# Kernel optimization log

Hardware: AMD Instinct MI355X
Metric: run time of the kernel (lower is better)

The kernel has to match this reference:

```python
import jax, jax.numpy as jnp
import numpy as np

Q_LORA = 1536
KV_LORA = 512
ROPE_DIM = 64
NOPE_DIM = 128
NUM_HEADS = 16
QK_HEAD_DIM = NOPE_DIM + ROPE_DIM  # 192
HEAD_SIZE = KV_LORA + ROPE_DIM     # 576
MAX_POS = 4096
ROPE_BASE = 10000.0
T = 32768


def _rope_cos_sin(positions):
    # inv_freq: [ROPE_DIM//2]
    inv_freq = 1.0 / (ROPE_BASE ** (jnp.arange(0, ROPE_DIM, 2, dtype=jnp.float32) / ROPE_DIM))
    freqs = positions.astype(jnp.float32)[:, None] * inv_freq[None, :]  # [T, D/2]
    return jnp.cos(freqs), jnp.sin(freqs)


def _apply_rope_neox(x, cos, sin):
    # x: [T, H, D]; cos/sin: [T, D/2] broadcast over heads
    x1, x2 = jnp.split(x, 2, axis=-1)
    c = cos[:, None, :]
    s = sin[:, None, :]
    return jnp.concatenate([x1 * c - x2 * s, x2 * c + x1 * s], axis=-1)


def setup_inputs() -> dict:
    key = jax.random.key(0)
    k1, k2, k3 = jax.random.split(key, 3)
    qkv_lora = jax.random.normal(k1, (T, Q_LORA + KV_LORA + ROPE_DIM), dtype=jnp.float32)
    positions = jax.random.randint(k2, (T,), 0, MAX_POS, dtype=jnp.int64)
    Wq = jax.random.normal(k3, (Q_LORA, NUM_HEADS * QK_HEAD_DIM), dtype=jnp.float32) * 0.02
    kv_cache = jnp.zeros((T, HEAD_SIZE), dtype=jnp.float32)
    slot_mapping = jnp.arange(T, dtype=jnp.int64)
    return {"qkv_lora": qkv_lora, "positions": positions, "Wq": Wq,
            "kv_cache": kv_cache, "slot_mapping": slot_mapping}


def reference(qkv_lora, positions, Wq, kv_cache, slot_mapping):
    # split low-rank projections
    q_c = qkv_lora[:, :Q_LORA]                               # [T, 1536]
    kv_c = qkv_lora[:, Q_LORA:Q_LORA + KV_LORA]              # [T, 512]
    k_pe = qkv_lora[:, Q_LORA + KV_LORA:]                    # [T, 64]

    # q_b_proj GEMM then reshape to heads
    q = (q_c @ Wq).reshape(T, NUM_HEADS, QK_HEAD_DIM)        # [T, H, 192]

    # RoPE on q rope slice and k_pe (neox style)
    cos, sin = _rope_cos_sin(positions)
    q_pe = _apply_rope_neox(q[..., NOPE_DIM:], cos, sin)     # [T, H, 64]
    k_pe_rot = _apply_rope_neox(k_pe[:, None, :], cos, sin)  # [T, 1, 64]
    q = jnp.concatenate([q[..., :NOPE_DIM], q_pe], axis=-1)

    # paged KV cache scatter write: concat(kv_c, k_pe) at slot_mapping
    entry = jnp.concatenate([kv_c, k_pe_rot[:, 0, :]], axis=-1)  # [T, 576]
    kv_cache = kv_cache.at[slot_mapping].set(entry)

    return q, kv_c, k_pe_rot, kv_cache
```

## Files before the change

kernel.cpp:

```cpp
#include <hip/hip_runtime.h>
#include <hip/hip_bf16.h>
#include <stdint.h>

typedef unsigned short ushort_t;
typedef __attribute__((ext_vector_type(4))) float f32x4;
typedef __attribute__((ext_vector_type(8))) short short8;

#define T_TOK 32768
#define QL    1536
#define KVL   512
#define RD    64
#define NQ    3072
#define ROWW  2112
#define HS    576

#define BM 256
#define BN 256
#define BK 64
#define KT (QL / BK)
#define MT (T_TOK / BM)
#define NT (NQ / BN)

#define NLOG (-0.28782313662425572f)

static __device__ __forceinline__ short f2bf(float x) {
  __hip_bfloat16 h = __float2bfloat16(x);
  return *reinterpret_cast<short*>(&h);
}

#define GLOAD16(gp, lp)                                        \
  __builtin_amdgcn_global_load_lds(                            \
      (const __attribute__((address_space(1))) void*)(gp),     \
      (__attribute__((address_space(3))) void*)(lp), 16, 0, 0)

__global__ __launch_bounds__(256) void aconv_kernel(const float* __restrict__ qkv,
                                                    ushort_t* __restrict__ Abf) {
  int g = blockIdx.x * 256 + threadIdx.x;
  int row = g / 192;
  int col = (g - row * 192) * 8;
  const float* s = qkv + (size_t)row * ROWW + col;
  f32x4 a = *(const f32x4*)s;
  f32x4 b = *(const f32x4*)(s + 4);
  short8 v;
  v[0] = f2bf(a[0]); v[1] = f2bf(a[1]); v[2] = f2bf(a[2]); v[3] = f2bf(a[3]);
  v[4] = f2bf(b[0]); v[5] = f2bf(b[1]); v[6] = f2bf(b[2]); v[7] = f2bf(b[3]);
  *(short8*)(Abf + (size_t)row * QL + col) = v;
}

__global__ void wq_t_kernel(const float* __restrict__ Wq, ushort_t* __restrict__ Wt) {
  __shared__ float tile[32][33];
  int tx = threadIdx.x, ty = threadIdx.y;
  int n0 = blockIdx.x * 32, k0 = blockIdx.y * 32;
#pragma unroll
  for (int j = 0; j < 32; j += 8)
    tile[ty + j][tx] = Wq[(size_t)(k0 + ty + j) * NQ + n0 + tx];
  __syncthreads();
#pragma unroll
  for (int j = 0; j < 32; j += 8)
    Wt[(size_t)(n0 + ty + j) * QL + k0 + tx] = f2bf(tile[tx][ty + j]);
}

__global__ __launch_bounds__(512, 2) void gemm_rope_kernel(
    const ushort_t* __restrict__ Abf, const int* __restrict__ pos,
    const ushort_t* __restrict__ wt, float* __restrict__ out_q) {
  __shared__ ushort_t lds[2][2][2][256 * 32];

  int bid = blockIdx.x;
  int vb = (bid & 7) * (MT * NT / 8) + (bid >> 3);
  int m0 = (vb / NT) * BM;
  int n0 = (vb % NT) * BN;

  int tid = threadIdx.x;
  int wv = tid >> 6, ln = tid & 63;
  int l16 = ln & 15, lq4 = ln >> 4;
  int wm = wv >> 2, wn = wv & 3;

  int srow = wv * 32 + (ln >> 2);
  int schunk = ((ln & 3) ^ ((ln >> 3) & 3)) * 8;
  const ushort_t* aS = Abf + (size_t)(m0 + srow) * QL + schunk;
  const ushort_t* bS = wt  + (size_t)(n0 + srow) * QL + schunk;
  int sdst = wv * 32 * 32;

#define STG(PAR, AB, KH, TT, SRC) do {                                         \
    GLOAD16((SRC) + (size_t)(TT) * BK + (KH) * 32,           &lds[PAR][AB][KH][sdst]);       \
    GLOAD16((SRC) + (size_t)(TT) * BK + (KH) * 32 + 16 * QL, &lds[PAR][AB][KH][sdst + 512]); \
  } while (0)

  int rkey = (l16 >> 1) & 3;
  int aoff = (wm * 128 + l16) * 32 + (lq4 ^ rkey) * 8;
  int boff = (wn * 64  + l16) * 32 + (lq4 ^ rkey) * 8;

  f32x4 acc[8][4];
#pragma unroll
  for (int i = 0; i < 8; ++i)
#pragma unroll
    for (int j = 0; j < 4; ++j) acc[i][j] = (f32x4)0.0f;

  STG(0, 0, 0, 0, aS);
  STG(0, 1, 0, 0, bS);
  STG(0, 0, 1, 0, aS);
  STG(0, 1, 1, 0, bS);
  STG(1, 0, 0, 1, aS);
  STG(1, 1, 0, 1, bS);

#define CLUSTER(ACCBASE, AF, BF)                                               \
  __builtin_amdgcn_s_setprio(1);                                               \
  _Pragma("unroll")                                                            \
  for (int q = 0; q < 4; ++q)                                                  \
    _Pragma("unroll")                                                          \
    for (int n = 0; n < 4; ++n)                                                \
      acc[(ACCBASE) + q][n] = __builtin_amdgcn_mfma_f32_16x16x32_bf16(         \
          AF[q], BF[n], acc[(ACCBASE) + q][n], 0, 0, 0);                       \
  __builtin_amdgcn_s_setprio(0);

#pragma unroll 2
  for (int t = 0; t < KT; ++t) {
    int par = t & 1;
    const ushort_t* Ak0 = &lds[par][0][0][0];
    const ushort_t* Bk0 = &lds[par][1][0][0];
    const ushort_t* Ak1 = &lds[par][0][1][0];
    const ushort_t* Bk1 = &lds[par][1][1][0];
    short8 af0[4], af1[4], bf0[4], ag0[4], ag1[4], bg0[4];

    __builtin_amdgcn_sched_barrier(0);
    if (t == KT - 1) { asm volatile("s_waitcnt vmcnt(0)" ::: "memory"); }
    else             { asm volatile("s_waitcnt vmcnt(4)" ::: "memory"); }
    __builtin_amdgcn_s_barrier();
    __builtin_amdgcn_sched_barrier(0);

#pragma unroll
    for (int q = 0; q < 4; ++q) af0[q] = *(const short8*)(Ak0 + aoff + q * 512);
#pragma unroll
    for (int n = 0; n < 4; ++n) bf0[n] = *(const short8*)(Bk0 + boff + n * 512);
#pragma unroll
    for (int q = 0; q < 4; ++q) af1[q] = *(const short8*)(Ak0 + aoff + (4 + q) * 512);
    if (t + 1 < KT) { STG(par ^ 1, 0, 1, t + 1, aS); STG(par ^ 1, 1, 1, t + 1, bS); }
#pragma unroll
    for (int q = 0; q < 4; ++q) ag0[q] = *(const short8*)(Ak1 + aoff + q * 512);
#pragma unroll
    for (int n = 0; n < 4; ++n) bg0[n] = *(const short8*)(Bk1 + boff + n * 512);
#pragma unroll
    for (int q = 0; q < 4; ++q) ag1[q] = *(const short8*)(Ak1 + aoff + (4 + q) * 512);
    __builtin_amdgcn_sched_barrier(0);

    CLUSTER(0, af0, bf0)
    CLUSTER(4, af1, bf0)

    __builtin_amdgcn_s_barrier();
    __builtin_amdgcn_sched_barrier(0);
    if (t + 2 < KT) { STG(par, 0, 0, t + 2, aS); STG(par, 1, 0, t + 2, bS); }

    CLUSTER(0, ag0, bg0)
    CLUSTER(4, ag1, bg0)
  }

  int gn = n0 + wn * 64;
  bool ropew = ((gn % 192) == 128);
  if (!ropew) {
#pragma unroll
    for (int mi = 0; mi < 8; ++mi)
#pragma unroll
      for (int r = 0; r < 4; ++r) {
        int t = m0 + wm * 128 + mi * 16 + lq4 * 4 + r;
        float* rowp = out_q + (size_t)t * NQ + gn + l16;
        rowp[0]  = acc[mi][0][r];
        rowp[16] = acc[mi][1][r];
        rowp[32] = acc[mi][2][r];
        rowp[48] = acc[mi][3][r];
      }
  } else {
    float invf0 = __expf((float)l16 * NLOG);
    float invf1 = __expf((float)(l16 + 16) * NLOG);
#pragma unroll
    for (int mi = 0; mi < 8; ++mi)
#pragma unroll
      for (int r = 0; r < 4; ++r) {
        int t = m0 + wm * 128 + mi * 16 + lq4 * 4 + r;
        float p = (float)pos[t];
        float s0, c0, s1, c1;
        __sincosf(p * invf0, &s0, &c0);
        __sincosf(p * invf1, &s1, &c1);
        float x1a = acc[mi][0][r], x1b = acc[mi][1][r];
        float x2a = acc[mi][2][r], x2b = acc[mi][3][r];
        float* rowp = out_q + (size_t)t * NQ + gn + l16;
        rowp[0]  = x1a * c0 - x2a * s0;
        rowp[16] = x1b * c1 - x2b * s1;
        rowp[32] = x2a * c0 + x1a * s0;
        rowp[48] = x2b * c1 + x1b * s1;
      }
  }
}

__global__ void kv_kernel(const float* __restrict__ qkv, const int* __restrict__ pos,
                          const int* __restrict__ slots,
                          float* __restrict__ out_kvc, float* __restrict__ out_kpe,
                          float* __restrict__ out_cache) {
  int tok = blockIdx.x * 4 + (threadIdx.x >> 6);
  int lane = threadIdx.x & 63;
  const float* src = qkv + (size_t)tok * ROWW + QL;
  float* dkv = out_kvc + (size_t)tok * KVL;
  int slot = slots[tok];
  float* dc = out_cache + (size_t)slot * HS;
#pragma unroll
  for (int i = 0; i < 2; ++i) {
    f32x4 v = *(const f32x4*)(src + (size_t)(lane + 64 * i) * 4);
    *(f32x4*)(dkv + (size_t)(lane + 64 * i) * 4) = v;
    *(f32x4*)(dc + (size_t)(lane + 64 * i) * 4) = v;
  }
  if (lane < 32) {
    float x1 = src[KVL + lane], x2 = src[KVL + 32 + lane];
    float p = (float)pos[tok];
    float invf = __expf((float)lane * NLOG);
    float s, c;
    __sincosf(p * invf, &s, &c);
    float r1 = x1 * c - x2 * s;
    float r2 = x2 * c + x1 * s;
    out_kpe[(size_t)tok * RD + lane] = r1;
    out_kpe[(size_t)tok * RD + 32 + lane] = r2;
    dc[KVL + lane] = r1;
    dc[KVL + 32 + lane] = r2;
  }
}

extern "C" void kernel_launch(void* const* d_in, const int* in_sizes, int n_in,
                              void* d_out, int out_size, void* d_ws, size_t ws_size,
                              hipStream_t stream) {
  const float* qkv       = (const float*)d_in[0];
  const int*   positions = (const int*)d_in[1];
  const float* Wq        = (const float*)d_in[2];
  const int*   slots     = (const int*)d_in[4];

  float* out_q     = (float*)d_out;
  float* out_kvc   = out_q   + (size_t)T_TOK * NQ;
  float* out_kpe   = out_kvc + (size_t)T_TOK * KVL;
  float* out_cache = out_kpe + (size_t)T_TOK * RD;

  size_t abf_bytes = (size_t)T_TOK * QL * sizeof(ushort_t);
  size_t wt_bytes  = (size_t)NQ * QL * sizeof(ushort_t);
  char* scratch = (ws_size >= abf_bytes + wt_bytes) ? (char*)d_ws : (char*)out_kvc;
  ushort_t* Abf = (ushort_t*)scratch;
  ushort_t* Wt  = (ushort_t*)(scratch + abf_bytes);

  aconv_kernel<<<dim3(T_TOK * 192 / 256), dim3(256), 0, stream>>>(qkv, Abf);
  wq_t_kernel<<<dim3(NQ / 32, QL / 32), dim3(32, 8), 0, stream>>>(Wq, Wt);
  gemm_rope_kernel<<<dim3(MT * NT), dim3(512), 0, stream>>>(Abf, positions, Wt, out_q);
  kv_kernel<<<dim3(T_TOK / 4), dim3(256), 0, stream>>>(qkv, positions, slots,
                                                       out_kvc, out_kpe, out_cache);
}
```

Baseline: 478.2 us.

## Merge prep kernels, fold KV cache write into GEMM epilogue, reorder LDS reads

```diff
diff --git a/kernel.cpp b/kernel.cpp
--- a/kernel.cpp
+++ b/kernel.cpp
@@ -21,6 +21,10 @@
 #define MT (T_TOK / BM)
 #define NT (NQ / BN)
 
+#define ACONV_BLOCKS (T_TOK * 192 / 256)
+#define WQ_BLOCKS    ((NQ / 32) * (QL / 32))
+#define KV_BLOCKS    1024
+
 #define NLOG (-0.28782313662425572f)
 
 static __device__ __forceinline__ short f2bf(float x) {
@@ -33,36 +37,43 @@
       (const __attribute__((address_space(1))) void*)(gp),     \
       (__attribute__((address_space(3))) void*)(lp), 16, 0, 0)
 
-__global__ __launch_bounds__(256) void aconv_kernel(const float* __restrict__ qkv,
-                                                    ushort_t* __restrict__ Abf) {
-  int g = blockIdx.x * 256 + threadIdx.x;
-  int row = g / 192;
-  int col = (g - row * 192) * 8;
-  const float* s = qkv + (size_t)row * ROWW + col;
-  f32x4 a = *(const f32x4*)s;
-  f32x4 b = *(const f32x4*)(s + 4);
-  short8 v;
-  v[0] = f2bf(a[0]); v[1] = f2bf(a[1]); v[2] = f2bf(a[2]); v[3] = f2bf(a[3]);
-  v[4] = f2bf(b[0]); v[5] = f2bf(b[1]); v[6] = f2bf(b[2]); v[7] = f2bf(b[3]);
-  *(short8*)(Abf + (size_t)row * QL + col) = v;
-}
-
-__global__ void wq_t_kernel(const float* __restrict__ Wq, ushort_t* __restrict__ Wt) {
+__global__ __launch_bounds__(256) void pre_kernel(const float* __restrict__ qkv,
+                                                  ushort_t* __restrict__ Abf,
+                                                  const float* __restrict__ Wq,
+                                                  ushort_t* __restrict__ Wt) {
   __shared__ float tile[32][33];
-  int tx = threadIdx.x, ty = threadIdx.y;
-  int n0 = blockIdx.x * 32, k0 = blockIdx.y * 32;
-#pragma unroll
-  for (int j = 0; j < 32; j += 8)
-    tile[ty + j][tx] = Wq[(size_t)(k0 + ty + j) * NQ + n0 + tx];
-  __syncthreads();
-#pragma unroll
-  for (int j = 0; j < 32; j += 8)
-    Wt[(size_t)(n0 + ty + j) * QL + k0 + tx] = f2bf(tile[tx][ty + j]);
+  int bid = blockIdx.x, tid = threadIdx.x;
+  if (bid < ACONV_BLOCKS) {
+    int g = bid * 256 + tid;
+    int row = g / 192;
+    int col = (g - row * 192) * 8;
+    const float* s = qkv + (size_t)row * ROWW + col;
+    f32x4 a = *(const f32x4*)s;
+    f32x4 b = *(const f32x4*)(s + 4);
+    short8 v;
+    v[0] = f2bf(a[0]); v[1] = f2bf(a[1]); v[2] = f2bf(a[2]); v[3] = f2bf(a[3]);
+    v[4] = f2bf(b[0]); v[5] = f2bf(b[1]); v[6] = f2bf(b[2]); v[7] = f2bf(b[3]);
+    *(short8*)(Abf + (size_t)row * QL + col) = v;
+  } else {
+    int b2 = bid - ACONV_BLOCKS;
+    int n0 = (b2 % (NQ / 32)) * 32, k0 = (b2 / (NQ / 32)) * 32;
+    int tx = tid & 31, ty = tid >> 5;
+#pragma unroll
+    for (int j = 0; j < 32; j += 8)
+      tile[ty + j][tx] = Wq[(size_t)(k0 + ty + j) * NQ + n0 + tx];
+    __syncthreads();
+#pragma unroll
+    for (int j = 0; j < 32; j += 8)
+      Wt[(size_t)(n0 + ty + j) * QL + k0 + tx] = f2bf(tile[tx][ty + j]);
+  }
 }
 
 __global__ __launch_bounds__(512, 2) void gemm_rope_kernel(
     const ushort_t* __restrict__ Abf, const int* __restrict__ pos,
-    const ushort_t* __restrict__ wt, float* __restrict__ out_q) {
+    const ushort_t* __restrict__ wt, float* __restrict__ out_q,
+    const float* __restrict__ qkv, const int* __restrict__ slots,
+    float* __restrict__ out_kvc, float* __restrict__ out_kpe,
+    float* __restrict__ out_cache, int fuse_kv) {
   __shared__ ushort_t lds[2][2][2][256 * 32];
 
   int bid = blockIdx.x;
@@ -135,17 +146,18 @@
 #pragma unroll
     for (int q = 0; q < 4; ++q) af1[q] = *(const short8*)(Ak0 + aoff + (4 + q) * 512);
     if (t + 1 < KT) { STG(par ^ 1, 0, 1, t + 1, aS); STG(par ^ 1, 1, 1, t + 1, bS); }
-#pragma unroll
-    for (int q = 0; q < 4; ++q) ag0[q] = *(const short8*)(Ak1 + aoff + q * 512);
-#pragma unroll
-    for (int n = 0; n < 4; ++n) bg0[n] = *(const short8*)(Bk1 + boff + n * 512);
-#pragma unroll
-    for (int q = 0; q < 4; ++q) ag1[q] = *(const short8*)(Ak1 + aoff + (4 + q) * 512);
-    __builtin_amdgcn_sched_barrier(0);
 
     CLUSTER(0, af0, bf0)
     CLUSTER(4, af1, bf0)
 
+#pragma unroll
+    for (int q = 0; q < 4; ++q) ag0[q] = *(const short8*)(Ak1 + aoff + q * 512);
+#pragma unroll
+    for (int n = 0; n < 4; ++n) bg0[n] = *(const short8*)(Bk1 + boff + n * 512);
+#pragma unroll
+    for (int q = 0; q < 4; ++q) ag1[q] = *(const short8*)(Ak1 + aoff + (4 + q) * 512);
+
+    __builtin_amdgcn_sched_barrier(0);
     __builtin_amdgcn_s_barrier();
     __builtin_amdgcn_sched_barrier(0);
     if (t + 2 < KT) { STG(par, 0, 0, t + 2, aS); STG(par, 1, 0, t + 2, bS); }
@@ -189,6 +201,35 @@
         rowp[48] = x2b * c1 + x1b * s1;
       }
   }
+
+  if (fuse_kv && bid < KV_BLOCKS) {
+#pragma unroll
+    for (int it = 0; it < 4; ++it) {
+      int tok = bid * 32 + wv * 4 + it;
+      const float* src = qkv + (size_t)tok * ROWW + QL;
+      float* dkv = out_kvc + (size_t)tok * KVL;
+      float* dc  = out_cache + (size_t)slots[tok] * HS;
+#pragma unroll
+      for (int i = 0; i < 2; ++i) {
+        f32x4 v = *(const f32x4*)(src + (size_t)(ln + 64 * i) * 4);
+        *(f32x4*)(dkv + (size_t)(ln + 64 * i) * 4) = v;
+        *(f32x4*)(dc + (size_t)(ln + 64 * i) * 4) = v;
+      }
+      if (ln < 32) {
+        float x1 = src[KVL + ln], x2 = src[KVL + 32 + ln];
+        float p = (float)pos[tok];
+        float invf = __expf((float)ln * NLOG);
+        float s, c;
+        __sincosf(p * invf, &s, &c);
+        float r1 = x1 * c - x2 * s;
+        float r2 = x2 * c + x1 * s;
+        out_kpe[(size_t)tok * RD + ln] = r1;
+        out_kpe[(size_t)tok * RD + 32 + ln] = r2;
+        dc[KVL + ln] = r1;
+        dc[KVL + 32 + ln] = r2;
+      }
+    }
+  }
 }
 
 __global__ void kv_kernel(const float* __restrict__ qkv, const int* __restrict__ pos,
@@ -199,8 +240,7 @@
   int lane = threadIdx.x & 63;
   const float* src = qkv + (size_t)tok * ROWW + QL;
   float* dkv = out_kvc + (size_t)tok * KVL;
-  int slot = slots[tok];
-  float* dc = out_cache + (size_t)slot * HS;
+  float* dc = out_cache + (size_t)slots[tok] * HS;
 #pragma unroll
   for (int i = 0; i < 2; ++i) {
     f32x4 v = *(const f32x4*)(src + (size_t)(lane + 64 * i) * 4);
@@ -237,13 +277,15 @@
 
   size_t abf_bytes = (size_t)T_TOK * QL * sizeof(ushort_t);
   size_t wt_bytes  = (size_t)NQ * QL * sizeof(ushort_t);
-  char* scratch = (ws_size >= abf_bytes + wt_bytes) ? (char*)d_ws : (char*)out_kvc;
+  int ws_ok = (ws_size >= abf_bytes + wt_bytes);
+  char* scratch = ws_ok ? (char*)d_ws : (char*)out_kvc;
   ushort_t* Abf = (ushort_t*)scratch;
   ushort_t* Wt  = (ushort_t*)(scratch + abf_bytes);
 
-  aconv_kernel<<<dim3(T_TOK * 192 / 256), dim3(256), 0, stream>>>(qkv, Abf);
-  wq_t_kernel<<<dim3(NQ / 32, QL / 32), dim3(32, 8), 0, stream>>>(Wq, Wt);
-  gemm_rope_kernel<<<dim3(MT * NT), dim3(512), 0, stream>>>(Abf, positions, Wt, out_q);
-  kv_kernel<<<dim3(T_TOK / 4), dim3(256), 0, stream>>>(qkv, positions, slots,
-                                                       out_kvc, out_kpe, out_cache);
-}
+  pre_kernel<<<dim3(ACONV_BLOCKS + WQ_BLOCKS), dim3(256), 0, stream>>>(qkv, Abf, Wq, Wt);
+  gemm_rope_kernel<<<dim3(MT * NT), dim3(512), 0, stream>>>(
+      Abf, positions, Wt, out_q, qkv, slots, out_kvc, out_kpe, out_cache, ws_ok);
+  if (!ws_ok)
+    kv_kernel<<<dim3(T_TOK / 4), dim3(256), 0, stream>>>(qkv, positions, slots,
+                                                         out_kvc, out_kpe, out_cache);
+}
```

Result: faster. 443.9 us (-7.2%).

## Merge preprocessing and KV kernels into one launch; defer second-half LDS fragment loads

Applied to the files above, without the earlier changes.

```diff
diff --git a/kernel.cpp b/kernel.cpp
--- a/kernel.cpp
+++ b/kernel.cpp
@@ -21,6 +21,10 @@
 #define MT (T_TOK / BM)
 #define NT (NQ / BN)
 
+#define ACONV_BLOCKS (T_TOK * 192 / 256)
+#define WQ_BLOCKS    ((NQ / 32) * (QL / 32))
+#define KVP_BLOCKS   (T_TOK / 4)
+
 #define NLOG (-0.28782313662425572f)
 
 static __device__ __forceinline__ short f2bf(float x) {
@@ -33,31 +37,69 @@
       (const __attribute__((address_space(1))) void*)(gp),     \
       (__attribute__((address_space(3))) void*)(lp), 16, 0, 0)
 
-__global__ __launch_bounds__(256) void aconv_kernel(const float* __restrict__ qkv,
-                                                    ushort_t* __restrict__ Abf) {
-  int g = blockIdx.x * 256 + threadIdx.x;
-  int row = g / 192;
-  int col = (g - row * 192) * 8;
-  const float* s = qkv + (size_t)row * ROWW + col;
-  f32x4 a = *(const f32x4*)s;
-  f32x4 b = *(const f32x4*)(s + 4);
-  short8 v;
-  v[0] = f2bf(a[0]); v[1] = f2bf(a[1]); v[2] = f2bf(a[2]); v[3] = f2bf(a[3]);
-  v[4] = f2bf(b[0]); v[5] = f2bf(b[1]); v[6] = f2bf(b[2]); v[7] = f2bf(b[3]);
-  *(short8*)(Abf + (size_t)row * QL + col) = v;
-}
-
-__global__ void wq_t_kernel(const float* __restrict__ Wq, ushort_t* __restrict__ Wt) {
+static __device__ __forceinline__ void kv_body(
+    int tok, int lane, const float* __restrict__ qkv, const int* __restrict__ pos,
+    const int* __restrict__ slots, float* __restrict__ out_kvc,
+    float* __restrict__ out_kpe, float* __restrict__ out_cache) {
+  const float* src = qkv + (size_t)tok * ROWW + QL;
+  float* dkv = out_kvc + (size_t)tok * KVL;
+  float* dc  = out_cache + (size_t)slots[tok] * HS;
+#pragma unroll
+  for (int i = 0; i < 2; ++i) {
+    f32x4 v = *(const f32x4*)(src + (size_t)(lane + 64 * i) * 4);
+    *(f32x4*)(dkv + (size_t)(lane + 64 * i) * 4) = v;
+    *(f32x4*)(dc + (size_t)(lane + 64 * i) * 4) = v;
+  }
+  if (lane < 32) {
+    float x1 = src[KVL + lane], x2 = src[KVL + 32 + lane];
+    float p = (float)pos[tok];
+    float invf = __expf((float)lane * NLOG);
+    float s, c;
+    __sincosf(p * invf, &s, &c);
+    float r1 = x1 * c - x2 * s;
+    float r2 = x2 * c + x1 * s;
+    out_kpe[(size_t)tok * RD + lane] = r1;
+    out_kpe[(size_t)tok * RD + 32 + lane] = r2;
+    dc[KVL + lane] = r1;
+    dc[KVL + 32 + lane] = r2;
+  }
+}
+
+__global__ __launch_bounds__(256) void pre_kernel(
+    const float* __restrict__ qkv, ushort_t* __restrict__ Abf,
+    const float* __restrict__ Wq, ushort_t* __restrict__ Wt,
+    const int* __restrict__ pos, const int* __restrict__ slots,
+    float* __restrict__ out_kvc, float* __restrict__ out_kpe,
+    float* __restrict__ out_cache, int do_kv) {
   __shared__ float tile[32][33];
-  int tx = threadIdx.x, ty = threadIdx.y;
-  int n0 = blockIdx.x * 32, k0 = blockIdx.y * 32;
-#pragma unroll
-  for (int j = 0; j < 32; j += 8)
-    tile[ty + j][tx] = Wq[(size_t)(k0 + ty + j) * NQ + n0 + tx];
-  __syncthreads();
-#pragma unroll
-  for (int j = 0; j < 32; j += 8)
-    Wt[(size_t)(n0 + ty + j) * QL + k0 + tx] = f2bf(tile[tx][ty + j]);
+  int bid = blockIdx.x, tid = threadIdx.x;
+  if (bid < ACONV_BLOCKS) {
+    int g = bid * 256 + tid;
+    int row = g / 192;
+    int col = (g - row * 192) * 8;
+    const float* s = qkv + (size_t)row * ROWW + col;
+    f32x4 a = *(const f32x4*)s;
+    f32x4 b = *(const f32x4*)(s + 4);
+    short8 v;
+    v[0] = f2bf(a[0]); v[1] = f2bf(a[1]); v[2] = f2bf(a[2]); v[3] = f2bf(a[3]);
+    v[4] = f2bf(b[0]); v[5] = f2bf(b[1]); v[6] = f2bf(b[2]); v[7] = f2bf(b[3]);
+    *(short8*)(Abf + (size_t)row * QL + col) = v;
+  } else if (bid < ACONV_BLOCKS + WQ_BLOCKS) {
+    int b2 = bid - ACONV_BLOCKS;
+    int n0 = (b2 % (NQ / 32)) * 32, k0 = (b2 / (NQ / 32)) * 32;
+    int tx = tid & 31, ty = tid >> 5;
+#pragma unroll
+    for (int j = 0; j < 32; j += 8)
+      tile[ty + j][tx] = Wq[(size_t)(k0 + ty + j) * NQ + n0 + tx];
+    __syncthreads();
+#pragma unroll
+    for (int j = 0; j < 32; j += 8)
+      Wt[(size_t)(n0 + ty + j) * QL + k0 + tx] = f2bf(tile[tx][ty + j]);
+  } else if (do_kv) {
+    int b3 = bid - ACONV_BLOCKS - WQ_BLOCKS;
+    int tok = b3 * 4 + (tid >> 6);
+    kv_body(tok, tid & 63, qkv, pos, slots, out_kvc, out_kpe, out_cache);
+  }
 }
 
 __global__ __launch_bounds__(512, 2) void gemm_rope_kernel(
@@ -135,17 +177,18 @@
 #pragma unroll
     for (int q = 0; q < 4; ++q) af1[q] = *(const short8*)(Ak0 + aoff + (4 + q) * 512);
     if (t + 1 < KT) { STG(par ^ 1, 0, 1, t + 1, aS); STG(par ^ 1, 1, 1, t + 1, bS); }
-#pragma unroll
-    for (int q = 0; q < 4; ++q) ag0[q] = *(const short8*)(Ak1 + aoff + q * 512);
-#pragma unroll
-    for (int n = 0; n < 4; ++n) bg0[n] = *(const short8*)(Bk1 + boff + n * 512);
-#pragma unroll
-    for (int q = 0; q < 4; ++q) ag1[q] = *(const short8*)(Ak1 + aoff + (4 + q) * 512);
-    __builtin_amdgcn_sched_barrier(0);
 
     CLUSTER(0, af0, bf0)
     CLUSTER(4, af1, bf0)
 
+#pragma unroll
+    for (int q = 0; q < 4; ++q) ag0[q] = *(const short8*)(Ak1 + aoff + q * 512);
+#pragma unroll
+    for (int n = 0; n < 4; ++n) bg0[n] = *(const short8*)(Bk1 + boff + n * 512);
+#pragma unroll
+    for (int q = 0; q < 4; ++q) ag1[q] = *(const short8*)(Ak1 + aoff + (4 + q) * 512);
+
+    __builtin_amdgcn_sched_barrier(0);
     __builtin_amdgcn_s_barrier();
     __builtin_amdgcn_sched_barrier(0);
     if (t + 2 < KT) { STG(par, 0, 0, t + 2, aS); STG(par, 1, 0, t + 2, bS); }
@@ -196,30 +239,7 @@
                           float* __restrict__ out_kvc, float* __restrict__ out_kpe,
                           float* __restrict__ out_cache) {
   int tok = blockIdx.x * 4 + (threadIdx.x >> 6);
-  int lane = threadIdx.x & 63;
-  const float* src = qkv + (size_t)tok * ROWW + QL;
-  float* dkv = out_kvc + (size_t)tok * KVL;
-  int slot = slots[tok];
-  float* dc = out_cache + (size_t)slot * HS;
-#pragma unroll
-  for (int i = 0; i < 2; ++i) {
-    f32x4 v = *(const f32x4*)(src + (size_t)(lane + 64 * i) * 4);
-    *(f32x4*)(dkv + (size_t)(lane + 64 * i) * 4) = v;
-    *(f32x4*)(dc + (size_t)(lane + 64 * i) * 4) = v;
-  }
-  if (lane < 32) {
-    float x1 = src[KVL + lane], x2 = src[KVL + 32 + lane];
-    float p = (float)pos[tok];
-    float invf = __expf((float)lane * NLOG);
-    float s, c;
-    __sincosf(p * invf, &s, &c);
-    float r1 = x1 * c - x2 * s;
-    float r2 = x2 * c + x1 * s;
-    out_kpe[(size_t)tok * RD + lane] = r1;
-    out_kpe[(size_t)tok * RD + 32 + lane] = r2;
-    dc[KVL + lane] = r1;
-    dc[KVL + 32 + lane] = r2;
-  }
+  kv_body(tok, threadIdx.x & 63, qkv, pos, slots, out_kvc, out_kpe, out_cache);
 }
 
 extern "C" void kernel_launch(void* const* d_in, const int* in_sizes, int n_in,
@@ -237,13 +257,16 @@
 
   size_t abf_bytes = (size_t)T_TOK * QL * sizeof(ushort_t);
   size_t wt_bytes  = (size_t)NQ * QL * sizeof(ushort_t);
-  char* scratch = (ws_size >= abf_bytes + wt_bytes) ? (char*)d_ws : (char*)out_kvc;
+  int ws_ok = (ws_size >= abf_bytes + wt_bytes);
+  char* scratch = ws_ok ? (char*)d_ws : (char*)out_kvc;
   ushort_t* Abf = (ushort_t*)scratch;
   ushort_t* Wt  = (ushort_t*)(scratch + abf_bytes);
 
-  aconv_kernel<<<dim3(T_TOK * 192 / 256), dim3(256), 0, stream>>>(qkv, Abf);
-  wq_t_kernel<<<dim3(NQ / 32, QL / 32), dim3(32, 8), 0, stream>>>(Wq, Wt);
+  int pre_blocks = ACONV_BLOCKS + WQ_BLOCKS + (ws_ok ? KVP_BLOCKS : 0);
+  pre_kernel<<<dim3(pre_blocks), dim3(256), 0, stream>>>(
+      qkv, Abf, Wq, Wt, positions, slots, out_kvc, out_kpe, out_cache, ws_ok);
   gemm_rope_kernel<<<dim3(MT * NT), dim3(512), 0, stream>>>(Abf, positions, Wt, out_q);
-  kv_kernel<<<dim3(T_TOK / 4), dim3(256), 0, stream>>>(qkv, positions, slots,
-                                                       out_kvc, out_kpe, out_cache);
-}
+  if (!ws_ok)
+    kv_kernel<<<dim3(KVP_BLOCKS), dim3(256), 0, stream>>>(qkv, positions, slots,
+                                                          out_kvc, out_kpe, out_cache);
+}
```

Result: faster. 431.9 us (-9.7%).
